# Optimization experiments

Hardware: AMD Instinct MI355X
Metric: run time of the kernel (lower is better)

The kernel has to match this reference:

```python
import jax, jax.numpy as jnp
import numpy as np

L, B, E, H = 2048, 2, 1024, 16
HD = E // H


def setup_inputs() -> dict:
    key = jax.random.key(0)
    ks = jax.random.split(key, 5)
    s = 0.02
    return {
        "query": jax.random.normal(ks[0], (L, B, E), jnp.float32),
        "key": jax.random.normal(ks[1], (L, B, E), jnp.float32),
        "value": jax.random.normal(ks[2], (L, B, E), jnp.float32),
        "in_proj_weight": jax.random.normal(ks[3], (3 * E, E), jnp.float32) * s,
        "in_proj_bias": jnp.zeros((3 * E,), jnp.float32),
        "out_proj_weight": jax.random.normal(ks[4], (E, E), jnp.float32) * s,
        "out_proj_bias": jnp.zeros((E,), jnp.float32),
    }


def reference(query, key, value, in_proj_weight, in_proj_bias, out_proj_weight, out_proj_bias):
    # torch nn.MultiheadAttention math, seq-first [L, B, E], causal mask
    # (attend_mode='only_attend_front': positions j > i are masked).
    w_q, w_k, w_v = jnp.split(in_proj_weight, 3, axis=0)
    b_q, b_k, b_v = jnpp_split(in_proj_bias) if False else jnp.split(in_proj_bias, 3, axis=0)
    q = query @ w_q.T + b_q            # [L, B, E]
    k = key @ w_k.T + b_k
    v = value @ w_v.T + b_v

    def heads(x):  # [L, B, E] -> [B, H, L, HD]
        return x.reshape(x.shape[0], x.shape[1], H, HD).transpose(1, 2, 0, 3)

    qh, kh, vh = heads(q), heads(k), heads(v)
    scale = 1.0 / jnp.sqrt(jnp.asarray(HD, q.dtype))
    scores = jnp.einsum("bhqd,bhkd->bhqk", qh * scale, kh)  # [B, H, L, L]
    causal = jnp.triu(jnp.ones((scores.shape[-2], scores.shape[-1]), bool), k=1)
    scores = jnp.where(causal, jnp.asarray(-jnp.inf, scores.dtype), scores)
    attn = jax.nn.softmax(scores, axis=-1)
    out = jnp.einsum("bhqk,bhkd->bhqd", attn, vh)           # [B, H, L, HD]
    out = out.transpose(2, 0, 1, 3).reshape(query.shape[0], query.shape[1], E)  # [L, B, E]
    out = out @ out_proj_weight.T + out_proj_bias
    # torch also returns head-averaged attn weights [B, L, L]
    attn_avg = attn.mean(axis=1)
    return out, attn_avg
```

## Files before the change

### kernel.cpp

```cpp
#include <hip/hip_runtime.h>

#define L_ 2048
#define B_ 2
#define E_ 1024
#define H_ 16
#define HD_ 64
#define M_ 4096
#define K_ 1024

typedef unsigned short u16;
typedef unsigned int u32;
using short8  = __attribute__((ext_vector_type(8))) short;
using short4v = __attribute__((ext_vector_type(4))) short;
using floatx4 = __attribute__((ext_vector_type(4))) float;

__device__ inline u16 f2b(float f) {
  unsigned u = __float_as_uint(f);
  u += 0x7FFF + ((u >> 16) & 1);
  return (u16)(u >> 16);
}

__device__ inline floatx4 mfma16(short8 a, short8 b, floatx4 c) {
  return __builtin_amdgcn_mfma_f32_16x16x32_bf16(a, b, c, 0, 0, 0);
}

__device__ inline void gload16(const void* g, void* l) {
  __builtin_amdgcn_global_load_lds(
      (const __attribute__((address_space(1))) u32*)g,
      (__attribute__((address_space(3))) u32*)l, 16, 0, 0);
}

__global__ void convk(const float* __restrict__ src, u16* __restrict__ dst, int n4) {
  int i = blockIdx.x * blockDim.x + threadIdx.x;
  if (i < n4) {
    float4 v = ((const float4*)src)[i];
    ushort4 o;
    o.x = f2b(v.x); o.y = f2b(v.y); o.z = f2b(v.z); o.w = f2b(v.w);
    ((ushort4*)dst)[i] = o;
  }
}

template <int MODE>
__global__ __launch_bounds__(256) void gemm128(
    const u16* __restrict__ A, const u16* __restrict__ W, const float* __restrict__ bias,
    u16* __restrict__ qh, u16* __restrict__ kh, u16* __restrict__ vhT,
    float* __restrict__ outp)
{
  __shared__ __align__(16) u16 As[128 * 32];
  __shared__ __align__(16) u16 Bs[128 * 32];
  const int p = (MODE == 0) ? blockIdx.z : 0;
  const u16* Ap = A + (size_t)p * M_ * K_;
  const u16* Wp = W + (size_t)p * E_ * K_;
  const float* bp = bias + p * E_;
  const int row0 = blockIdx.y * 128, col0 = blockIdx.x * 128;
  const int t = threadIdx.x, lane = t & 63, wv = t >> 6;
  const int lanem = lane & 15, quad = lane >> 4;
  const int wm = wv >> 1, wn = wv & 1;

  int f0 = t, f1 = 256 + t;
  int r0s = f0 >> 2, q0s = (f0 & 3) ^ ((r0s >> 1) & 3);
  int r1s = f1 >> 2, q1s = (f1 & 3) ^ ((r1s >> 1) & 3);

  floatx4 acc[4][4];
#pragma unroll
  for (int mi = 0; mi < 4; ++mi)
#pragma unroll
    for (int ni = 0; ni < 4; ++ni) acc[mi][ni] = (floatx4){0.f, 0.f, 0.f, 0.f};

  const int swz = (lanem >> 1) & 3;

  for (int k0 = 0; k0 < K_; k0 += 32) {
    __syncthreads();
    gload16(Ap + (size_t)(row0 + r0s) * K_ + k0 + q0s * 8, (char*)As + wv * 1024);
    gload16(Wp + (size_t)(col0 + r0s) * K_ + k0 + q0s * 8, (char*)Bs + wv * 1024);
    gload16(Ap + (size_t)(row0 + r1s) * K_ + k0 + q1s * 8, (char*)As + 4096 + wv * 1024);
    gload16(Wp + (size_t)(col0 + r1s) * K_ + k0 + q1s * 8, (char*)Bs + 4096 + wv * 1024);
    __syncthreads();
    short8 af[4], bfg[4];
#pragma unroll
    for (int mi = 0; mi < 4; ++mi) {
      int r = wm * 64 + mi * 16 + lanem;
      af[mi] = *(const short8*)((const char*)As + r * 64 + (quad ^ swz) * 16);
    }
#pragma unroll
    for (int ni = 0; ni < 4; ++ni) {
      int r = wn * 64 + ni * 16 + lanem;
      bfg[ni] = *(const short8*)((const char*)Bs + r * 64 + (quad ^ swz) * 16);
    }
#pragma unroll
    for (int mi = 0; mi < 4; ++mi)
#pragma unroll
      for (int ni = 0; ni < 4; ++ni)
        acc[mi][ni] = mfma16(af[mi], bfg[ni], acc[mi][ni]);
  }

#pragma unroll
  for (int ni = 0; ni < 4; ++ni) {
    int gc = col0 + wn * 64 + ni * 16 + lanem;
    float bv = bp[gc];
#pragma unroll
    for (int mi = 0; mi < 4; ++mi) {
      int gr0 = row0 + wm * 64 + mi * 16 + quad * 4;
#pragma unroll
      for (int v = 0; v < 4; ++v) {
        float val = acc[mi][ni][v] + bv;
        int r = gr0 + v;
        if (MODE == 1) {
          outp[(size_t)r * E_ + gc] = val;
        } else {
          int l = r >> 1, bb = r & 1, hh = gc >> 6, d = gc & 63;
          u16 x = f2b(val);
          if (p == 0)      qh[(((size_t)bb * H_ + hh) * L_ + l) * HD_ + d] = x;
          else if (p == 1) kh[(((size_t)bb * H_ + hh) * L_ + l) * HD_ + d] = x;
          else             vhT[(((size_t)bb * H_ + hh) * HD_ + d) * L_ + l] = x;
        }
      }
    }
  }
}

__global__ __launch_bounds__(256) void attn1(
    const u16* __restrict__ qh, const u16* __restrict__ kh, const u16* __restrict__ vhT,
    u16* __restrict__ ctx, float* __restrict__ li_ws)
{
  __shared__ __align__(16) u16 Ks[64 * 64];
  __shared__ __align__(16) u16 Vs[64 * 64];
  const int it = (L_ / 64 - 1) - blockIdx.x;
  const int h = blockIdx.y, b = blockIdx.z;
  const int t = threadIdx.x, lane = t & 63, wv = t >> 6;
  const int lanem = lane & 15, quad = lane >> 4;
  const int bh = b * H_ + h;
  const int i0 = it * 64 + wv * 16;
  const int irow = i0 + lanem;

  const u16* qb = qh + ((size_t)bh * L_ + irow) * HD_;
  short8 qa0 = *(const short8*)(qb + quad * 8);
  short8 qa1 = *(const short8*)(qb + 32 + quad * 8);

  const int srow = lane >> 3;
  const int spiece = (lane & 7) ^ srow;
  const u16* kgbase = kh + (size_t)bh * L_ * HD_;
  const u16* vgbase = vhT + (size_t)bh * HD_ * L_;

  float li = 0.f;
  floatx4 o[4];
#pragma unroll
  for (int d = 0; d < 4; ++d) o[d] = (floatx4){0.f, 0.f, 0.f, 0.f};

  const int swz = lanem & 7;
  const int nj = it + 1;

  for (int jt = 0; jt < nj; ++jt) {
    const int j0 = jt * 64;
    __syncthreads();
#pragma unroll
    for (int k = wv * 2; k < wv * 2 + 2; ++k) {
      int r = k * 8 + srow;
      gload16(kgbase + (size_t)(j0 + r) * HD_ + spiece * 8, (char*)Ks + k * 1024);
      gload16(vgbase + (size_t)r * L_ + j0 + spiece * 8, (char*)Vs + k * 1024);
    }
    __syncthreads();

    floatx4 st[4];
#pragma unroll
    for (int jf = 0; jf < 4; ++jf) {
      const char* kr = (const char*)Ks + (jf * 16 + lanem) * 128;
      short8 a0 = *(const short8*)(kr + ((quad) ^ swz) * 16);
      short8 a1 = *(const short8*)(kr + ((4 + quad) ^ swz) * 16);
      floatx4 s = (floatx4){0.f, 0.f, 0.f, 0.f};
      s = mfma16(a0, qa0, s);
      s = mfma16(a1, qa1, s);
      st[jf] = s;
    }

    short8 pb[2];
    if (j0 + 63 <= i0) {
#pragma unroll
      for (int jc = 0; jc < 2; ++jc)
#pragma unroll
        for (int r = 0; r < 4; ++r) {
          float p0 = __expf(st[jc * 2][r] * 0.125f);
          float p1 = __expf(st[jc * 2 + 1][r] * 0.125f);
          li += p0 + p1;
          pb[jc][r] = (short)f2b(p0);
          pb[jc][4 + r] = (short)f2b(p1);
        }
    } else {
#pragma unroll
      for (int jc = 0; jc < 2; ++jc)
#pragma unroll
        for (int r = 0; r < 4; ++r) {
          int ja = j0 + jc * 32 + quad * 4 + r;
          int jb2 = ja + 16;
          float p0 = (ja <= irow) ? __expf(st[jc * 2][r] * 0.125f) : 0.f;
          float p1 = (jb2 <= irow) ? __expf(st[jc * 2 + 1][r] * 0.125f) : 0.f;
          li += p0 + p1;
          pb[jc][r] = (short)f2b(p0);
          pb[jc][4 + r] = (short)f2b(p1);
        }
    }

#pragma unroll
    for (int jc = 0; jc < 2; ++jc) {
      int p0 = jc * 4 + (quad >> 1), p1 = p0 + 2;
#pragma unroll
      for (int dbl = 0; dbl < 4; ++dbl) {
        const char* vr = (const char*)Vs + (dbl * 16 + lanem) * 128 + (quad & 1) * 8;
        short8 vf;
        ((short4v*)&vf)[0] = *(const short4v*)(vr + (p0 ^ swz) * 16);
        ((short4v*)&vf)[1] = *(const short4v*)(vr + (p1 ^ swz) * 16);
        o[dbl] = mfma16(vf, pb[jc], o[dbl]);
      }
    }
  }

  li += __shfl_xor(li, 16);
  li += __shfl_xor(li, 32);
  float inv = 1.0f / li;

  u16* cb = ctx + ((size_t)irow * B_ + b) * E_ + h * HD_ + quad * 4;
#pragma unroll
  for (int dbl = 0; dbl < 4; ++dbl) {
    ushort4 pk;
    pk.x = f2b(o[dbl][0] * inv);
    pk.y = f2b(o[dbl][1] * inv);
    pk.z = f2b(o[dbl][2] * inv);
    pk.w = f2b(o[dbl][3] * inv);
    *(ushort4*)(cb + dbl * 16) = pk;
  }
  if (quad == 0) li_ws[(size_t)bh * L_ + irow] = inv;
}

__global__ __launch_bounds__(256) void attn2(
    const u16* __restrict__ qh, const u16* __restrict__ kh,
    const float* __restrict__ li_ws, float* __restrict__ out2)
{
  __shared__ __align__(16) u16 Ks[2][2][64 * 64];
  const int jt = blockIdx.x, it = blockIdx.y, b = blockIdx.z;
  const int t = threadIdx.x, lane = t & 63, wv = t >> 6;
  const int lanem = lane & 15, quad = lane >> 4;
  const int i0 = it * 64 + wv * 16;
  const int j0 = jt * 64;
  float* ob = out2 + (size_t)b * L_ * L_;

  if (jt > it) {
    float4 z = {0.f, 0.f, 0.f, 0.f};
    float* rp = ob + (size_t)(i0 + lanem) * L_ + j0 + quad * 16;
    ((float4*)rp)[0] = z; ((float4*)rp)[1] = z;
    ((float4*)rp)[2] = z; ((float4*)rp)[3] = z;
    return;
  }

  const int srow = lane >> 3;
  const int spiece = (lane & 7) ^ srow;
  const int swz = lanem & 7;

  auto stage = [&](int p, int buf) {
#pragma unroll
    for (int hh = 0; hh < 2; ++hh) {
      const u16* kg = kh + ((size_t)(b * H_ + 2 * p + hh) * L_ + j0) * HD_;
#pragma unroll
      for (int k = wv * 2; k < wv * 2 + 2; ++k)
        gload16(kg + (size_t)(k * 8 + srow) * HD_ + spiece * 8,
                (char*)Ks[buf][hh] + k * 1024);
    }
  };
  auto loadQ = [&](int p, short8 q[2][2], floatx4 lf[2]) {
#pragma unroll
    for (int hh = 0; hh < 2; ++hh) {
      int bh = b * H_ + 2 * p + hh;
      const u16* qb = qh + ((size_t)bh * L_ + i0 + lanem) * HD_;
      q[hh][0] = *(const short8*)(qb + quad * 8);
      q[hh][1] = *(const short8*)(qb + 32 + quad * 8);
      lf[hh] = *(const floatx4*)(li_ws + (size_t)bh * L_ + i0 + quad * 4);
    }
  };

  float acc[4][4] = {};
  short8 qc[2][2]; floatx4 lc[2];
  stage(0, 0);
  loadQ(0, qc, lc);

#pragma unroll
  for (int p = 0; p < 8; ++p) {
    const int buf = p & 1;
    if (p < 7) stage(p + 1, 1 - buf);
    __syncthreads();
    short8 qn[2][2]; floatx4 ln[2];
    loadQ(p < 7 ? p + 1 : 7, qn, ln);
#pragma unroll
    for (int hh = 0; hh < 2; ++hh) {
      const char* tb = (const char*)Ks[buf][hh];
#pragma unroll
      for (int s = 0; s < 4; ++s) {
        if (j0 + s * 16 > i0 + 15) continue;
        const char* kr = tb + (s * 16 + lanem) * 128;
        short8 b0 = *(const short8*)(kr + (quad ^ swz) * 16);
        short8 b1 = *(const short8*)(kr + ((4 + quad) ^ swz) * 16);
        floatx4 sv = (floatx4){0.f, 0.f, 0.f, 0.f};
        sv = mfma16(qc[hh][0], b0, sv);
        sv = mfma16(qc[hh][1], b1, sv);
        if (j0 + s * 16 + 15 <= i0) {
#pragma unroll
          for (int r = 0; r < 4; ++r)
            acc[s][r] += __expf(sv[r] * 0.125f) * lc[hh][r];
        } else {
#pragma unroll
          for (int r = 0; r < 4; ++r) {
            int irow = i0 + quad * 4 + r;
            int jc = j0 + s * 16 + lanem;
            if (jc <= irow) acc[s][r] += __expf(sv[r] * 0.125f) * lc[hh][r];
          }
        }
      }
    }
#pragma unroll
    for (int hh = 0; hh < 2; ++hh) {
      qc[hh][0] = qn[hh][0]; qc[hh][1] = qn[hh][1]; lc[hh] = ln[hh];
    }
  }

#pragma unroll
  for (int s = 0; s < 4; ++s)
#pragma unroll
    for (int r = 0; r < 4; ++r) {
      int irow = i0 + quad * 4 + r;
      int jc = j0 + s * 16 + lanem;
      ob[(size_t)irow * L_ + jc] = acc[s][r] * (1.0f / H_);
    }
}

extern "C" void kernel_launch(void* const* d_in, const int* in_sizes, int n_in,
                              void* d_out, int out_size, void* d_ws, size_t ws_size,
                              hipStream_t stream) {
  const float* query = (const float*)d_in[0];
  const float* key   = (const float*)d_in[1];
  const float* value = (const float*)d_in[2];
  const float* w_in  = (const float*)d_in[3];
  const float* b_in  = (const float*)d_in[4];
  const float* w_out = (const float*)d_in[5];
  const float* b_out = (const float*)d_in[6];

  char* ws = (char*)d_ws;
  size_t off = 0;
  auto alloc = [&](size_t bytes) -> void* {
    void* p = ws + off;
    off += (bytes + 255) & ~(size_t)255;
    return p;
  };
  u16* w_in_b  = (u16*)alloc((size_t)3 * E_ * K_ * 2);
  u16* w_out_b = (u16*)alloc((size_t)E_ * K_ * 2);
  u16* x_b     = (u16*)alloc((size_t)3 * M_ * K_ * 2);
  u16* qh      = (u16*)alloc((size_t)B_ * H_ * L_ * HD_ * 2);
  u16* kh      = (u16*)alloc((size_t)B_ * H_ * L_ * HD_ * 2);
  u16* vhT     = (u16*)alloc((size_t)B_ * H_ * L_ * HD_ * 2);
  u16* ctx     = (u16*)alloc((size_t)M_ * E_ * 2);
  float* li_ws = (float*)alloc((size_t)B_ * H_ * L_ * 4);

  convk<<<4096, 256, 0, stream>>>(query, x_b + (size_t)0 * M_ * K_, M_ * K_ / 4);
  convk<<<4096, 256, 0, stream>>>(key,   x_b + (size_t)1 * M_ * K_, M_ * K_ / 4);
  convk<<<4096, 256, 0, stream>>>(value, x_b + (size_t)2 * M_ * K_, M_ * K_ / 4);
  convk<<<3072, 256, 0, stream>>>(w_in,  w_in_b,  3 * E_ * K_ / 4);
  convk<<<1024, 256, 0, stream>>>(w_out, w_out_b, E_ * K_ / 4);

  gemm128<0><<<dim3(E_ / 128, M_ / 128, 3), 256, 0, stream>>>(
      x_b, w_in_b, b_in, qh, kh, vhT, nullptr);

  attn1<<<dim3(L_ / 64, H_, B_), 256, 0, stream>>>(qh, kh, vhT, ctx, li_ws);

  attn2<<<dim3(L_ / 64, L_ / 64, B_), 256, 0, stream>>>(
      qh, kh, li_ws, (float*)d_out + (size_t)M_ * E_);

  gemm128<1><<<dim3(E_ / 128, M_ / 128, 1), 256, 0, stream>>>(
      ctx, w_out_b, b_out, nullptr, nullptr, nullptr, (float*)d_out);
}
```

Measured before the change: 304.8 us.

## Process two query tiles per attention block and permute V layout for wide LDS reads

Each attn1 block now handles 128 query rows, split into two 64-row halves that share every loaded K/V tile. This halves the K/V global-to-LDS traffic and the number of sync rounds per row. The V projection output is stored with a permuted sequence index so each V fragment comes from one 16-byte LDS read instead of two 8-byte reads. Other changes are a cheaper round-half-up bf16 pack, precomputed LDS offsets, and a 4-waves occupancy hint. The cost is more registers, fewer blocks (less parallelism), and slightly different bf16 rounding.

```diff
diff --git a/kernel.cpp b/kernel.cpp
--- a/kernel.cpp
+++ b/kernel.cpp
@@ -18,6 +18,12 @@
   unsigned u = __float_as_uint(f);
   u += 0x7FFF + ((u >> 16) & 1);
   return (u16)(u >> 16);
+}
+
+__device__ inline u32 pack2(float a, float b) {
+  u32 ua = __float_as_uint(a) + 0x8000u;
+  u32 ub = __float_as_uint(b) + 0x8000u;
+  return (ua >> 16) | (ub & 0xFFFF0000u);
 }
 
 __device__ inline floatx4 mfma16(short8 a, short8 b, floatx4 c) {
@@ -112,123 +118,142 @@
           u16 x = f2b(val);
           if (p == 0)      qh[(((size_t)bb * H_ + hh) * L_ + l) * HD_ + d] = x;
           else if (p == 1) kh[(((size_t)bb * H_ + hh) * L_ + l) * HD_ + d] = x;
-          else             vhT[(((size_t)bb * H_ + hh) * HD_ + d) * L_ + l] = x;
+          else {
+            int lp = (l & ~31) | (((l >> 2) & 3) * 8 + ((l >> 4) & 1) * 4 + (l & 3));
+            vhT[(((size_t)bb * H_ + hh) * HD_ + d) * L_ + lp] = x;
+          }
         }
       }
     }
   }
 }
 
-__global__ __launch_bounds__(256) void attn1(
+__global__ __launch_bounds__(256, 4) void attn1(
     const u16* __restrict__ qh, const u16* __restrict__ kh, const u16* __restrict__ vhT,
     u16* __restrict__ ctx, float* __restrict__ li_ws)
 {
   __shared__ __align__(16) u16 Ks[64 * 64];
   __shared__ __align__(16) u16 Vs[64 * 64];
-  const int it = (L_ / 64 - 1) - blockIdx.x;
+  const int it = (L_ / 128 - 1) - blockIdx.x;
   const int h = blockIdx.y, b = blockIdx.z;
   const int t = threadIdx.x, lane = t & 63, wv = t >> 6;
   const int lanem = lane & 15, quad = lane >> 4;
   const int bh = b * H_ + h;
-  const int i0 = it * 64 + wv * 16;
-  const int irow = i0 + lanem;
-
-  const u16* qb = qh + ((size_t)bh * L_ + irow) * HD_;
-  short8 qa0 = *(const short8*)(qb + quad * 8);
-  short8 qa1 = *(const short8*)(qb + 32 + quad * 8);
+  const int i0 = it * 128;
+  const int baseA = i0 + wv * 16;
+  const int baseB = i0 + 64 + wv * 16;
+  const int rowA = baseA + lanem, rowB = baseB + lanem;
+
+  const u16* qpA = qh + ((size_t)bh * L_ + rowA) * HD_;
+  const u16* qpB = qh + ((size_t)bh * L_ + rowB) * HD_;
+  short8 qA0 = *(const short8*)(qpA + quad * 8);
+  short8 qA1 = *(const short8*)(qpA + 32 + quad * 8);
+  short8 qB0 = *(const short8*)(qpB + quad * 8);
+  short8 qB1 = *(const short8*)(qpB + 32 + quad * 8);
 
   const int srow = lane >> 3;
   const int spiece = (lane & 7) ^ srow;
-  const u16* kgbase = kh + (size_t)bh * L_ * HD_;
-  const u16* vgbase = vhT + (size_t)bh * HD_ * L_;
-
-  float li = 0.f;
-  floatx4 o[4];
-#pragma unroll
-  for (int d = 0; d < 4; ++d) o[d] = (floatx4){0.f, 0.f, 0.f, 0.f};
+  const u16* ksrc = kh + ((size_t)bh * L_ + wv * 16 + srow) * HD_ + spiece * 8;
+  const u16* vsrc = vhT + ((size_t)bh * HD_ + wv * 16 + srow) * L_ + spiece * 8;
+  char* kdst = (char*)Ks + wv * 2048;
+  char* vdst = (char*)Vs + wv * 2048;
 
   const int swz = lanem & 7;
-  const int nj = it + 1;
-
-  for (int jt = 0; jt < nj; ++jt) {
-    const int j0 = jt * 64;
+  const int cb0 = lanem * 128 + ((quad ^ swz)) * 16;
+  const int cb1 = lanem * 128 + ((quad ^ swz) ^ 4) * 16;
+
+  float liA = 0.f, liB = 0.f;
+  floatx4 oA[4], oB[4];
+#pragma unroll
+  for (int d = 0; d < 4; ++d) { oA[d] = (floatx4){0.f,0.f,0.f,0.f}; oB[d] = oA[d]; }
+
+  int j0 = 0;
+
+  auto do_tile = [&](int modeA, int modeB) {
     __syncthreads();
-#pragma unroll
-    for (int k = wv * 2; k < wv * 2 + 2; ++k) {
-      int r = k * 8 + srow;
-      gload16(kgbase + (size_t)(j0 + r) * HD_ + spiece * 8, (char*)Ks + k * 1024);
-      gload16(vgbase + (size_t)r * L_ + j0 + spiece * 8, (char*)Vs + k * 1024);
-    }
+    gload16(ksrc, kdst);
+    gload16(ksrc + 8 * HD_, kdst + 1024);
+    gload16(vsrc, vdst);
+    gload16(vsrc + (size_t)8 * L_, vdst + 1024);
+    ksrc += 64 * HD_;
+    vsrc += 64;
     __syncthreads();
 
-    floatx4 st[4];
+    floatx4 sA[4], sB[4];
 #pragma unroll
     for (int jf = 0; jf < 4; ++jf) {
-      const char* kr = (const char*)Ks + (jf * 16 + lanem) * 128;
-      short8 a0 = *(const short8*)(kr + ((quad) ^ swz) * 16);
-      short8 a1 = *(const short8*)(kr + ((4 + quad) ^ swz) * 16);
-      floatx4 s = (floatx4){0.f, 0.f, 0.f, 0.f};
-      s = mfma16(a0, qa0, s);
-      s = mfma16(a1, qa1, s);
-      st[jf] = s;
-    }
-
-    short8 pb[2];
-    if (j0 + 63 <= i0) {
-#pragma unroll
-      for (int jc = 0; jc < 2; ++jc)
-#pragma unroll
-        for (int r = 0; r < 4; ++r) {
-          float p0 = __expf(st[jc * 2][r] * 0.125f);
-          float p1 = __expf(st[jc * 2 + 1][r] * 0.125f);
-          li += p0 + p1;
-          pb[jc][r] = (short)f2b(p0);
-          pb[jc][4 + r] = (short)f2b(p1);
-        }
-    } else {
-#pragma unroll
-      for (int jc = 0; jc < 2; ++jc)
+      short8 a0 = *(const short8*)((const char*)Ks + cb0 + jf * 2048);
+      short8 a1 = *(const short8*)((const char*)Ks + cb1 + jf * 2048);
+      floatx4 z = (floatx4){0.f,0.f,0.f,0.f};
+      if (modeA != 2) sA[jf] = mfma16(a1, qA1, mfma16(a0, qA0, z));
+      sB[jf] = mfma16(a1, qB1, mfma16(a0, qB0, z));
+    }
+
+    short8 pbA[2], pbB[2];
+    auto soft = [&](floatx4* st, int row, float& li, short8* pb, int masked) {
+#pragma unroll
+      for (int jc = 0; jc < 2; ++jc) {
+        float p[8];
 #pragma unroll
         for (int r = 0; r < 4; ++r) {
           int ja = j0 + jc * 32 + quad * 4 + r;
-          int jb2 = ja + 16;
-          float p0 = (ja <= irow) ? __expf(st[jc * 2][r] * 0.125f) : 0.f;
-          float p1 = (jb2 <= irow) ? __expf(st[jc * 2 + 1][r] * 0.125f) : 0.f;
-          li += p0 + p1;
-          pb[jc][r] = (short)f2b(p0);
-          pb[jc][4 + r] = (short)f2b(p1);
+          float e0 = __expf(st[jc * 2][r] * 0.125f);
+          float e1 = __expf(st[jc * 2 + 1][r] * 0.125f);
+          if (masked) {
+            e0 = (ja <= row) ? e0 : 0.f;
+            e1 = (ja + 16 <= row) ? e1 : 0.f;
+          }
+          li += e0 + e1;
+          p[r] = e0; p[4 + r] = e1;
         }
-    }
+        union { u32 w[4]; short8 s; } u;
+        u.w[0] = pack2(p[0], p[1]); u.w[1] = pack2(p[2], p[3]);
+        u.w[2] = pack2(p[4], p[5]); u.w[3] = pack2(p[6], p[7]);
+        pb[jc] = u.s;
+      }
+    };
+    if (modeA == 0) soft(sA, rowA, liA, pbA, 0);
+    else if (modeA == 1) soft(sA, rowA, liA, pbA, 1);
+    if (modeB == 0) soft(sB, rowB, liB, pbB, 0);
+    else soft(sB, rowB, liB, pbB, 1);
 
 #pragma unroll
     for (int jc = 0; jc < 2; ++jc) {
-      int p0 = jc * 4 + (quad >> 1), p1 = p0 + 2;
+      const int base = (jc == 0) ? cb0 : cb1;
 #pragma unroll
       for (int dbl = 0; dbl < 4; ++dbl) {
-        const char* vr = (const char*)Vs + (dbl * 16 + lanem) * 128 + (quad & 1) * 8;
-        short8 vf;
-        ((short4v*)&vf)[0] = *(const short4v*)(vr + (p0 ^ swz) * 16);
-        ((short4v*)&vf)[1] = *(const short4v*)(vr + (p1 ^ swz) * 16);
-        o[dbl] = mfma16(vf, pb[jc], o[dbl]);
+        short8 vf = *(const short8*)((const char*)Vs + base + dbl * 2048);
+        if (modeA != 2) oA[dbl] = mfma16(vf, pbA[jc], oA[dbl]);
+        oB[dbl] = mfma16(vf, pbB[jc], oB[dbl]);
       }
     }
-  }
-
-  li += __shfl_xor(li, 16);
-  li += __shfl_xor(li, 32);
-  float inv = 1.0f / li;
-
-  u16* cb = ctx + ((size_t)irow * B_ + b) * E_ + h * HD_ + quad * 4;
+    j0 += 64;
+  };
+
+  for (int jt = 0; jt < 2 * it; ++jt) do_tile(0, 0);
+  do_tile(1, 0);
+  do_tile(2, 1);
+
+  liA += __shfl_xor(liA, 16); liA += __shfl_xor(liA, 32);
+  liB += __shfl_xor(liB, 16); liB += __shfl_xor(liB, 32);
+  float invA = 1.0f / liA, invB = 1.0f / liB;
+
+  u16* cA = ctx + ((size_t)rowA * B_ + b) * E_ + h * HD_ + quad * 4;
+  u16* cB = ctx + ((size_t)rowB * B_ + b) * E_ + h * HD_ + quad * 4;
 #pragma unroll
   for (int dbl = 0; dbl < 4; ++dbl) {
-    ushort4 pk;
-    pk.x = f2b(o[dbl][0] * inv);
-    pk.y = f2b(o[dbl][1] * inv);
-    pk.z = f2b(o[dbl][2] * inv);
-    pk.w = f2b(o[dbl][3] * inv);
-    *(ushort4*)(cb + dbl * 16) = pk;
-  }
-  if (quad == 0) li_ws[(size_t)bh * L_ + irow] = inv;
+    ushort4 pkA, pkB;
+    pkA.x = f2b(oA[dbl][0] * invA); pkA.y = f2b(oA[dbl][1] * invA);
+    pkA.z = f2b(oA[dbl][2] * invA); pkA.w = f2b(oA[dbl][3] * invA);
+    pkB.x = f2b(oB[dbl][0] * invB); pkB.y = f2b(oB[dbl][1] * invB);
+    pkB.z = f2b(oB[dbl][2] * invB); pkB.w = f2b(oB[dbl][3] * invB);
+    *(ushort4*)(cA + dbl * 16) = pkA;
+    *(ushort4*)(cB + dbl * 16) = pkB;
+  }
+  if (quad == 0) {
+    li_ws[(size_t)bh * L_ + rowA] = invA;
+    li_ws[(size_t)bh * L_ + rowB] = invB;
+  }
 }
 
 __global__ __launch_bounds__(256) void attn2(
@@ -366,7 +391,7 @@
   gemm128<0><<<dim3(E_ / 128, M_ / 128, 3), 256, 0, stream>>>(
       x_b, w_in_b, b_in, qh, kh, vhT, nullptr);
 
-  attn1<<<dim3(L_ / 64, H_, B_), 256, 0, stream>>>(qh, kh, vhT, ctx, li_ws);
+  attn1<<<dim3(L_ / 128, H_, B_), 256, 0, stream>>>(qh, kh, vhT, ctx, li_ws);
 
   attn2<<<dim3(L_ / 64, L_ / 64, B_), 256, 0, stream>>>(
       qh, kh, li_ws, (float*)d_out + (size_t)M_ * E_);
```

Result: faster. 286.6 us (-6.0%).
